# Kernel tuning notes

Hardware: AMD Instinct MI355X
Metric: run time of the kernel (lower is better)

Reference implementation:

```python
import jax, jax.numpy as jnp
import numpy as np

N, C_IN, F = 64, 1024, 20          # batch, backbone channels, grid size (640/32)
N_CLASSES = 80
A = 3                               # anchors in this layer (mask [6,7,8])
STRIDE = 32
C = N_CLASSES + 5                   # 85
C_OUT = A * C                       # 255
ANCHORS = np.array([[116.0, 90.0], [156.0, 198.0], [373.0, 326.0]], np.float32) / STRIDE


def setup_inputs() -> dict:
    key = jax.random.key(0)
    k1, k2 = jax.random.split(key)
    xin = jax.random.normal(k1, (N, C_IN, F, F), jnp.float32)
    conv_w = jax.random.normal(k2, (C_OUT, C_IN, 1, 1), jnp.float32) * 0.02
    conv_b = jnp.zeros((C_OUT,), jnp.float32)
    return {"xin": xin, "conv_w": conv_w, "conv_b": conv_b}


def reference(xin, conv_w, conv_b):
    anchors = jnp.asarray(ANCHORS, dtype=xin.dtype)  # [A, 2], grid units
    # 1x1 conv head: [N, C_OUT, F, F]
    out = jax.lax.conv_general_dilated(xin, conv_w, window_strides=(1, 1),
                                       padding="VALID")
    out = out + conv_b[None, :, None, None]
    # [N, A, C, F, F] -> [N, A, F(y), F(x), C]
    out = out.reshape(N, A, C, F, F).transpose(0, 1, 3, 4, 2)

    xy = jax.nn.sigmoid(out[..., :2])       # sigmoid on tx, ty
    wh = out[..., 2:4]                      # raw tw, th
    objcls = jax.nn.sigmoid(out[..., 4:])   # sigmoid on obj + classes

    grid = jnp.arange(F, dtype=xin.dtype)
    px = xy[..., 0] + grid[None, None, None, :]   # + x_shift (varies along last spatial dim)
    py = xy[..., 1] + grid[None, None, :, None]   # + y_shift
    pw = jnp.exp(wh[..., 0]) * anchors[:, 0].reshape(1, A, 1, 1)
    ph = jnp.exp(wh[..., 1]) * anchors[:, 1].reshape(1, A, 1, 1)

    boxes = jnp.stack([px, py, pw, ph], axis=-1) * STRIDE  # back to pixel coords
    pred = jnp.concatenate([boxes, objcls], axis=-1)       # [N, A, F, F, C]
    return pred.reshape(N, -1, C)                           # [N, A*F*F, C]
```

## Files before the change

kernel.cpp:

```cpp
#include <hip/hip_runtime.h>
#include <hip/hip_bf16.h>
#include <math.h>

#define CIN    1024
#define S_TOT  400
#define COUT   255
#define NCH    85
#define NIMG   64
#define BM     256
#define BN     80
#define BK     64
#define NSTEP  (CIN / BK)
#define NTHR   512

#define XS_BASE   32768
#define LDS_BYTES (32768 + 10240)
#define WSTEP_B   32768

typedef __attribute__((ext_vector_type(8))) short bf16x8;
typedef __attribute__((ext_vector_type(4))) float f32x4;

__device__ __forceinline__ int wOff(int co, int kg) {
    return (co << 7) + ((kg << 4) ^ ((co & 7) << 4));
}
__device__ __forceinline__ int xOff(int s, int kg) {
    return XS_BASE + (s << 7) + ((kg << 4) ^ (((s >> 1) & 7) << 4));
}

__device__ __forceinline__ unsigned pk2(float a, float b) {
    __hip_bfloat162 h;
    h.x = __float2bfloat16(a);
    h.y = __float2bfloat16(b);
    return *reinterpret_cast<unsigned*>(&h);
}

__device__ __forceinline__ float sigmoidf_(float v) {
    return 1.0f / (1.0f + expf(-v));
}

__device__ __forceinline__ void gload_lds16(const void* g, void* l) {
    __builtin_amdgcn_global_load_lds(
        (const __attribute__((address_space(1))) unsigned int*)g,
        (__attribute__((address_space(3))) unsigned int*)l,
        16, 0, 0);
}

__global__ __launch_bounds__(256) void w_pre(const float* __restrict__ w,
                                             unsigned short* __restrict__ wbf) {
    int g = blockIdx.x * 256 + threadIdx.x;
    int co    = g >> 7;
    int kgAll = g & 127;
    int k     = kgAll << 3;
    int step  = k >> 6;
    int kg    = (k >> 3) & 7;
    union { unsigned short u[8]; bf16x8 v; } pk;
    if (co < COUT) {
        const float* src = w + co * CIN + k;
        #pragma unroll
        for (int j = 0; j < 8; ++j) {
            __hip_bfloat16 h = __float2bfloat16(src[j]);
            pk.u[j] = *reinterpret_cast<unsigned short*>(&h);
        }
    } else {
        #pragma unroll
        for (int j = 0; j < 8; ++j) pk.u[j] = 0;
    }
    char* dst = reinterpret_cast<char*>(wbf) + step * WSTEP_B + wOff(co, kg);
    *reinterpret_cast<bf16x8*>(dst) = pk.v;
}

__global__ __launch_bounds__(NTHR) void yolo_mfma(
    const float* __restrict__ xin,
    const unsigned short* __restrict__ wbf,
    const float* __restrict__ bias,
    float* __restrict__ out)
{
    __shared__ __align__(16) char smem[LDS_BYTES];

    const int n     = blockIdx.y;
    const int sbase = blockIdx.x * BN;
    const int tid   = threadIdx.x;
    const int lane  = tid & 63;
    const int wid   = tid >> 6;

    const float* xin_n = xin + (size_t)n * (CIN * S_TOT);

    const bool xstage = tid < 320;
    const int  sp = tid % 40;
    const int  kg = tid / 40;
    const int  s0 = sp * 2;
    const float* xsrc0 = xin_n + (kg * 8) * S_TOT + sbase + s0;

    f32x4 acc[2][5] = {};

    float2 cur[8], nxt[8];
    if (xstage) {
        #pragma unroll
        for (int j = 0; j < 8; ++j) cur[j] = *(const float2*)(xsrc0 + j * S_TOT);
    }

    const int co_w = wid * 32;
    const int llo  = lane & 15;
    const int lhi  = lane >> 4;

    for (int t = 0; t < NSTEP; ++t) {
        const char* wg = (const char*)wbf + (size_t)t * WSTEP_B;
        #pragma unroll
        for (int i = 0; i < 4; ++i) {
            gload_lds16(wg + i * 8192 + (size_t)tid * 16,
                        smem + i * 8192 + wid * 1024);
        }

        if (xstage) {
            union { unsigned u[4]; bf16x8 v; } r0, r1;
            #pragma unroll
            for (int j = 0; j < 4; ++j) {
                r0.u[j] = pk2(cur[2 * j].x, cur[2 * j + 1].x);
                r1.u[j] = pk2(cur[2 * j].y, cur[2 * j + 1].y);
            }
            *(bf16x8*)(smem + xOff(s0,     kg)) = r0.v;
            *(bf16x8*)(smem + xOff(s0 + 1, kg)) = r1.v;
        }
        __syncthreads();

        if (t + 1 < NSTEP && xstage) {
            const float* src = xsrc0 + (t + 1) * BK * S_TOT;
            #pragma unroll
            for (int j = 0; j < 8; ++j) nxt[j] = *(const float2*)(src + j * S_TOT);
        }

        #pragma unroll
        for (int ks = 0; ks < 2; ++ks) {
            const int kgr = ks * 4 + lhi;
            bf16x8 a0 = *(bf16x8*)(smem + wOff(co_w + llo,      kgr));
            bf16x8 a1 = *(bf16x8*)(smem + wOff(co_w + 16 + llo, kgr));
            #pragma unroll
            for (int ni = 0; ni < 5; ++ni) {
                bf16x8 b = *(bf16x8*)(smem + xOff(ni * 16 + llo, kgr));
                acc[0][ni] = __builtin_amdgcn_mfma_f32_16x16x32_bf16(a0, b, acc[0][ni], 0, 0, 0);
                acc[1][ni] = __builtin_amdgcn_mfma_f32_16x16x32_bf16(a1, b, acc[1][ni], 0, 0, 0);
            }
        }
        __syncthreads();

        if (xstage) {
            #pragma unroll
            for (int j = 0; j < 8; ++j) cur[j] = nxt[j];
        }
    }

    const float anchW[3] = {116.0f, 156.0f, 373.0f};
    const float anchH[3] = {90.0f, 198.0f, 326.0f};

    #pragma unroll
    for (int mi = 0; mi < 2; ++mi) {
        #pragma unroll
        for (int r = 0; r < 4; ++r) {
            int co = co_w + mi * 16 + lhi * 4 + r;
            if (co < COUT) {
                int a = co / NCH;
                int c = co - a * NCH;
                float bv = bias[co];
                #pragma unroll
                for (int ni = 0; ni < 5; ++ni) {
                    int s = sbase + ni * 16 + llo;
                    float v = acc[mi][ni][r] + bv;
                    float res;
                    if (c == 0)      res = (sigmoidf_(v) + (float)(s % 20)) * 32.0f;
                    else if (c == 1) res = (sigmoidf_(v) + (float)(s / 20)) * 32.0f;
                    else if (c == 2) res = expf(v) * anchW[a];
                    else if (c == 3) res = expf(v) * anchH[a];
                    else             res = sigmoidf_(v);
                    out[(size_t)n * 102000 + a * 34000 + s * 85 + c] = res;
                }
            }
        }
    }
}

extern "C" void kernel_launch(void* const* d_in, const int* in_sizes, int n_in,
                              void* d_out, int out_size, void* d_ws, size_t ws_size,
                              hipStream_t stream) {
    const float* xin  = (const float*)d_in[0];
    const float* w    = (const float*)d_in[1];
    const float* bias = (const float*)d_in[2];
    float* out = (float*)d_out;
    unsigned short* wbf = (unsigned short*)d_ws;

    w_pre<<<128, 256, 0, stream>>>(w, wbf);
    yolo_mfma<<<dim3(S_TOT / BN, NIMG), NTHR, 0, stream>>>(xin, wbf, bias, out);
}
```

Measured before the change: 74.03 us.

## Double-buffer weight tiles in LDS and prefetch activations two steps ahead

The K loop is unrolled by two and uses two LDS weight buffers. The async global-to-LDS weight load for the next step is issued before the current step computes, and activation registers are prefetched two steps ahead in alternating register sets. Manual vmcnt/lgkmcnt waits and raw s_barrier calls replace __syncthreads, and launch bounds add an occupancy hint. The aim is to hide global load latency behind the MFMA work. In exchange the kernel uses more LDS and registers, which may reduce resident blocks per CU, and it depends on hand-counted outstanding-load numbers being right.

```diff
diff --git a/kernel.cpp b/kernel.cpp
--- a/kernel.cpp
+++ b/kernel.cpp
@@ -7,15 +7,16 @@
 #define COUT   255
 #define NCH    85
 #define NIMG   64
-#define BM     256
 #define BN     80
 #define BK     64
-#define NSTEP  (CIN / BK)
+#define NSTEP  16
 #define NTHR   512
 
-#define XS_BASE   32768
-#define LDS_BYTES (32768 + 10240)
-#define WSTEP_B   32768
+#define WB0      0
+#define WB1      32768
+#define XS_BASE  65536
+#define LDS_BYTES (65536 + 10240)
+#define WSTEP_B  32768
 
 typedef __attribute__((ext_vector_type(8))) short bf16x8;
 typedef __attribute__((ext_vector_type(4))) float f32x4;
@@ -69,7 +70,52 @@
     *reinterpret_cast<bf16x8*>(dst) = pk.v;
 }
 
-__global__ __launch_bounds__(NTHR) void yolo_mfma(
+#define PHASE(T, CURB, NXTB, RC)                                               \
+  {                                                                            \
+    __builtin_amdgcn_sched_barrier(0);                                         \
+    const int tn  = ((T) + 1 < NSTEP) ? (T) + 1 : NSTEP - 1;                   \
+    const int tn2 = ((T) + 2 < NSTEP) ? (T) + 2 : NSTEP - 1;                   \
+    const char* wg_ = (const char*)wbf + (size_t)tn * WSTEP_B;                 \
+    _Pragma("unroll")                                                          \
+    for (int i = 0; i < 4; ++i)                                                \
+      gload_lds16(wg_ + i * 8192 + (size_t)tid * 16,                           \
+                  smem + (NXTB) + i * 8192 + wid * 1024);                      \
+    __builtin_amdgcn_sched_barrier(0);                                         \
+    if (xstage) {                                                              \
+      union { unsigned u[4]; bf16x8 v; } r0_, r1_;                             \
+      _Pragma("unroll")                                                        \
+      for (int j = 0; j < 4; ++j) {                                            \
+        r0_.u[j] = pk2(RC[2 * j].x, RC[2 * j + 1].x);                          \
+        r1_.u[j] = pk2(RC[2 * j].y, RC[2 * j + 1].y);                          \
+      }                                                                        \
+      *(bf16x8*)(smem + xOff(s0, kg))     = r0_.v;                             \
+      *(bf16x8*)(smem + xOff(s0 + 1, kg)) = r1_.v;                             \
+      const float* xs_ = xsrc0 + (size_t)tn2 * (BK * S_TOT);                   \
+      _Pragma("unroll")                                                        \
+      for (int j = 0; j < 8; ++j) RC[j] = *(const float2*)(xs_ + j * S_TOT);   \
+    }                                                                          \
+    asm volatile("s_waitcnt lgkmcnt(0)" ::: "memory");                         \
+    if (xstage) asm volatile("s_waitcnt vmcnt(20)" ::: "memory");              \
+    else        asm volatile("s_waitcnt vmcnt(4)"  ::: "memory");              \
+    __builtin_amdgcn_s_barrier();                                              \
+    __builtin_amdgcn_sched_barrier(0);                                         \
+    _Pragma("unroll")                                                          \
+    for (int ks = 0; ks < 2; ++ks) {                                           \
+      const int kgr = ks * 4 + lhi;                                            \
+      bf16x8 a0 = *(bf16x8*)(smem + (CURB) + wOff(co_w + llo,      kgr));      \
+      bf16x8 a1 = *(bf16x8*)(smem + (CURB) + wOff(co_w + 16 + llo, kgr));      \
+      _Pragma("unroll")                                                        \
+      for (int ni = 0; ni < 5; ++ni) {                                         \
+        bf16x8 b = *(bf16x8*)(smem + xOff(ni * 16 + llo, kgr));                \
+        acc[0][ni] = __builtin_amdgcn_mfma_f32_16x16x32_bf16(a0, b, acc[0][ni], 0, 0, 0); \
+        acc[1][ni] = __builtin_amdgcn_mfma_f32_16x16x32_bf16(a1, b, acc[1][ni], 0, 0, 0); \
+      }                                                                        \
+    }                                                                          \
+    __builtin_amdgcn_sched_barrier(0);                                         \
+    __builtin_amdgcn_s_barrier();                                              \
+  }
+
+__global__ __launch_bounds__(NTHR, 4) void yolo_mfma(
     const float* __restrict__ xin,
     const unsigned short* __restrict__ wbf,
     const float* __restrict__ bias,
@@ -93,59 +139,40 @@
 
     f32x4 acc[2][5] = {};
 
-    float2 cur[8], nxt[8];
-    if (xstage) {
-        #pragma unroll
-        for (int j = 0; j < 8; ++j) cur[j] = *(const float2*)(xsrc0 + j * S_TOT);
-    }
-
     const int co_w = wid * 32;
     const int llo  = lane & 15;
     const int lhi  = lane >> 4;
 
-    for (int t = 0; t < NSTEP; ++t) {
-        const char* wg = (const char*)wbf + (size_t)t * WSTEP_B;
-        #pragma unroll
-        for (int i = 0; i < 4; ++i) {
-            gload_lds16(wg + i * 8192 + (size_t)tid * 16,
-                        smem + i * 8192 + wid * 1024);
-        }
-
-        if (xstage) {
-            union { unsigned u[4]; bf16x8 v; } r0, r1;
-            #pragma unroll
-            for (int j = 0; j < 4; ++j) {
-                r0.u[j] = pk2(cur[2 * j].x, cur[2 * j + 1].x);
-                r1.u[j] = pk2(cur[2 * j].y, cur[2 * j + 1].y);
-            }
-            *(bf16x8*)(smem + xOff(s0,     kg)) = r0.v;
-            *(bf16x8*)(smem + xOff(s0 + 1, kg)) = r1.v;
-        }
-        __syncthreads();
-
-        if (t + 1 < NSTEP && xstage) {
-            const float* src = xsrc0 + (t + 1) * BK * S_TOT;
-            #pragma unroll
-            for (int j = 0; j < 8; ++j) nxt[j] = *(const float2*)(src + j * S_TOT);
-        }
-
-        #pragma unroll
-        for (int ks = 0; ks < 2; ++ks) {
-            const int kgr = ks * 4 + lhi;
-            bf16x8 a0 = *(bf16x8*)(smem + wOff(co_w + llo,      kgr));
-            bf16x8 a1 = *(bf16x8*)(smem + wOff(co_w + 16 + llo, kgr));
-            #pragma unroll
-            for (int ni = 0; ni < 5; ++ni) {
-                bf16x8 b = *(bf16x8*)(smem + xOff(ni * 16 + llo, kgr));
-                acc[0][ni] = __builtin_amdgcn_mfma_f32_16x16x32_bf16(a0, b, acc[0][ni], 0, 0, 0);
-                acc[1][ni] = __builtin_amdgcn_mfma_f32_16x16x32_bf16(a1, b, acc[1][ni], 0, 0, 0);
-            }
-        }
-        __syncthreads();
-
-        if (xstage) {
-            #pragma unroll
-            for (int j = 0; j < 8; ++j) cur[j] = nxt[j];
+    float2 XE[8], XO[8];
+    if (xstage) {
+        #pragma unroll
+        for (int j = 0; j < 8; ++j) XE[j] = *(const float2*)(xsrc0 + j * S_TOT);
+    }
+    __builtin_amdgcn_sched_barrier(0);
+    {
+        const char* wg_ = (const char*)wbf;
+        #pragma unroll
+        for (int i = 0; i < 4; ++i)
+            gload_lds16(wg_ + i * 8192 + (size_t)tid * 16,
+                        smem + WB0 + i * 8192 + wid * 1024);
+    }
+    __builtin_amdgcn_sched_barrier(0);
+    if (xstage) {
+        const float* xs1 = xsrc0 + BK * S_TOT;
+        #pragma unroll
+        for (int j = 0; j < 8; ++j) XO[j] = *(const float2*)(xs1 + j * S_TOT);
+    }
+
+    for (int it = 0; it < NSTEP; it += 2) {
+        PHASE(it,     WB0, WB1, XE);
+        PHASE(it + 1, WB1, WB0, XO);
+    }
+
+    if (xstage) {
+        #pragma unroll
+        for (int j = 0; j < 8; ++j) {
+            asm volatile("" :: "v"(XE[j].x), "v"(XE[j].y));
+            asm volatile("" :: "v"(XO[j].x), "v"(XO[j].y));
         }
     }
 
```

After: 70.05 us. 5.4% less time.

## Split output channels across two blocks and vectorize epilogue stores

Applied to the files above, without the earlier changes.

The 255 output channels are split across two blocks of 256 threads each, replacing one 512-thread block that owned all channels, and launch bounds ask for 4 blocks per CU. The register double-buffering of the activation tile is dropped in favour of direct load-convert-store each step. The epilogue writes four consecutive channels with one 16-byte store when they fall in the same anchor. The aim is more resident blocks and fewer scattered stores. The cost is that every activation tile is read twice, and global load latency is no longer overlapped within the block.

```diff
diff --git a/kernel.cpp b/kernel.cpp
--- a/kernel.cpp
+++ b/kernel.cpp
@@ -7,18 +7,19 @@
 #define COUT   255
 #define NCH    85
 #define NIMG   64
-#define BM     256
 #define BN     80
 #define BK     64
-#define NSTEP  (CIN / BK)
-#define NTHR   512
-
-#define XS_BASE   32768
-#define LDS_BYTES (32768 + 10240)
+#define NSTEP  16
+#define NTHR   256
+
+#define XS_BASE   16384
+#define LDS_BYTES (16384 + 10240)
 #define WSTEP_B   32768
 
 typedef __attribute__((ext_vector_type(8))) short bf16x8;
 typedef __attribute__((ext_vector_type(4))) float f32x4;
+
+struct __attribute__((aligned(4))) f4u { float x, y, z, w; };
 
 __device__ __forceinline__ int wOff(int co, int kg) {
     return (co << 7) + ((kg << 4) ^ ((co & 7) << 4));
@@ -69,7 +70,21 @@
     *reinterpret_cast<bf16x8*>(dst) = pk.v;
 }
 
-__global__ __launch_bounds__(NTHR) void yolo_mfma(
+__device__ __forceinline__ void stageX(const float* base, char* smem, int s0, int kg) {
+    float2 cu[8];
+    #pragma unroll
+    for (int j = 0; j < 8; ++j) cu[j] = *(const float2*)(base + j * S_TOT);
+    union { unsigned u[4]; bf16x8 v; } r0, r1;
+    #pragma unroll
+    for (int j = 0; j < 4; ++j) {
+        r0.u[j] = pk2(cu[2 * j].x, cu[2 * j + 1].x);
+        r1.u[j] = pk2(cu[2 * j].y, cu[2 * j + 1].y);
+    }
+    *(bf16x8*)(smem + xOff(s0,     kg)) = r0.v;
+    *(bf16x8*)(smem + xOff(s0 + 1, kg)) = r1.v;
+}
+
+__global__ __launch_bounds__(NTHR, 4) void yolo_mfma(
     const float* __restrict__ xin,
     const unsigned short* __restrict__ wbf,
     const float* __restrict__ bias,
@@ -77,7 +92,8 @@
 {
     __shared__ __align__(16) char smem[LDS_BYTES];
 
-    const int n     = blockIdx.y;
+    const int n     = blockIdx.z;
+    const int cob   = blockIdx.y * 128;
     const int sbase = blockIdx.x * BN;
     const int tid   = threadIdx.x;
     const int lane  = tid & 63;
@@ -85,49 +101,31 @@
 
     const float* xin_n = xin + (size_t)n * (CIN * S_TOT);
 
-    const bool xstage = tid < 320;
-    const int  sp = tid % 40;
-    const int  kg = tid / 40;
-    const int  s0 = sp * 2;
-    const float* xsrc0 = xin_n + (kg * 8) * S_TOT + sbase + s0;
+    const int kg0 = tid / 40;
+    const int sp0 = tid % 40;
+    const int kg1 = (256 + tid) / 40;
+    const int sp1 = (256 + tid) % 40;
+    const bool dual = tid < 64;
 
     f32x4 acc[2][5] = {};
-
-    float2 cur[8], nxt[8];
-    if (xstage) {
-        #pragma unroll
-        for (int j = 0; j < 8; ++j) cur[j] = *(const float2*)(xsrc0 + j * S_TOT);
-    }
 
     const int co_w = wid * 32;
     const int llo  = lane & 15;
     const int lhi  = lane >> 4;
 
     for (int t = 0; t < NSTEP; ++t) {
-        const char* wg = (const char*)wbf + (size_t)t * WSTEP_B;
-        #pragma unroll
-        for (int i = 0; i < 4; ++i) {
-            gload_lds16(wg + i * 8192 + (size_t)tid * 16,
-                        smem + i * 8192 + wid * 1024);
-        }
-
-        if (xstage) {
-            union { unsigned u[4]; bf16x8 v; } r0, r1;
-            #pragma unroll
-            for (int j = 0; j < 4; ++j) {
-                r0.u[j] = pk2(cur[2 * j].x, cur[2 * j + 1].x);
-                r1.u[j] = pk2(cur[2 * j].y, cur[2 * j + 1].y);
-            }
-            *(bf16x8*)(smem + xOff(s0,     kg)) = r0.v;
-            *(bf16x8*)(smem + xOff(s0 + 1, kg)) = r1.v;
-        }
+        const char* wg = (const char*)wbf + (size_t)t * WSTEP_B + (size_t)cob * 128;
+        #pragma unroll
+        for (int i = 0; i < 4; ++i)
+            gload_lds16(wg + i * 4096 + (size_t)tid * 16,
+                        smem + i * 4096 + wid * 1024);
+
+        const float* xt = xin_n + (size_t)t * (BK * S_TOT) + sbase;
+        stageX(xt + kg0 * 8 * S_TOT + 2 * sp0, smem, 2 * sp0, kg0);
+        if (dual)
+            stageX(xt + kg1 * 8 * S_TOT + 2 * sp1, smem, 2 * sp1, kg1);
+
         __syncthreads();
-
-        if (t + 1 < NSTEP && xstage) {
-            const float* src = xsrc0 + (t + 1) * BK * S_TOT;
-            #pragma unroll
-            for (int j = 0; j < 8; ++j) nxt[j] = *(const float2*)(src + j * S_TOT);
-        }
 
         #pragma unroll
         for (int ks = 0; ks < 2; ++ks) {
@@ -142,11 +140,6 @@
             }
         }
         __syncthreads();
-
-        if (xstage) {
-            #pragma unroll
-            for (int j = 0; j < 8; ++j) cur[j] = nxt[j];
-        }
     }
 
     const float anchW[3] = {116.0f, 156.0f, 373.0f};
@@ -154,24 +147,53 @@
 
     #pragma unroll
     for (int mi = 0; mi < 2; ++mi) {
-        #pragma unroll
-        for (int r = 0; r < 4; ++r) {
-            int co = co_w + mi * 16 + lhi * 4 + r;
-            if (co < COUT) {
-                int a = co / NCH;
-                int c = co - a * NCH;
-                float bv = bias[co];
+        const int co0 = cob + co_w + mi * 16 + lhi * 4;
+        const int aW  = co0 / NCH;
+        const int c0  = co0 - aW * NCH;
+        const bool whole = (c0 <= NCH - 4) && (co0 + 3 < COUT);
+        float bv[4];
+        #pragma unroll
+        for (int r = 0; r < 4; ++r)
+            bv[r] = (co0 + r < COUT) ? bias[co0 + r] : 0.0f;
+
+        #pragma unroll
+        for (int ni = 0; ni < 5; ++ni) {
+            const int s  = sbase + ni * 16 + llo;
+            const float sx = (float)(s % 20);
+            const float sy = (float)(s / 20);
+            if (whole) {
+                float r4[4];
                 #pragma unroll
-                for (int ni = 0; ni < 5; ++ni) {
-                    int s = sbase + ni * 16 + llo;
-                    float v = acc[mi][ni][r] + bv;
+                for (int r = 0; r < 4; ++r) {
+                    const int c = c0 + r;
+                    const float v = acc[mi][ni][r] + bv[r];
                     float res;
-                    if (c == 0)      res = (sigmoidf_(v) + (float)(s % 20)) * 32.0f;
-                    else if (c == 1) res = (sigmoidf_(v) + (float)(s / 20)) * 32.0f;
-                    else if (c == 2) res = expf(v) * anchW[a];
-                    else if (c == 3) res = expf(v) * anchH[a];
+                    if (c == 0)      res = (sigmoidf_(v) + sx) * 32.0f;
+                    else if (c == 1) res = (sigmoidf_(v) + sy) * 32.0f;
+                    else if (c == 2) res = expf(v) * anchW[aW];
+                    else if (c == 3) res = expf(v) * anchH[aW];
                     else             res = sigmoidf_(v);
-                    out[(size_t)n * 102000 + a * 34000 + s * 85 + c] = res;
+                    r4[r] = res;
+                }
+                f4u* p = (f4u*)(out + (size_t)n * 102000 + aW * 34000 + s * 85 + c0);
+                f4u val = {r4[0], r4[1], r4[2], r4[3]};
+                *p = val;
+            } else {
+                #pragma unroll
+                for (int r = 0; r < 4; ++r) {
+                    const int co = co0 + r;
+                    if (co < COUT) {
+                        const int a2 = co / NCH;
+                        const int c  = co - a2 * NCH;
+                        const float v = acc[mi][ni][r] + bv[r];
+                        float res;
+                        if (c == 0)      res = (sigmoidf_(v) + sx) * 32.0f;
+                        else if (c == 1) res = (sigmoidf_(v) + sy) * 32.0f;
+                        else if (c == 2) res = expf(v) * anchW[a2];
+                        else if (c == 3) res = expf(v) * anchH[a2];
+                        else             res = sigmoidf_(v);
+                        out[(size_t)n * 102000 + a2 * 34000 + s * 85 + c] = res;
+                    }
                 }
             }
         }
@@ -188,5 +210,5 @@
     unsigned short* wbf = (unsigned short*)d_ws;
 
     w_pre<<<128, 256, 0, stream>>>(w, wbf);
-    yolo_mfma<<<dim3(S_TOT / BN, NIMG), NTHR, 0, stream>>>(xin, wbf, bias, out);
-}
+    yolo_mfma<<<dim3(S_TOT / BN, 2, NIMG), NTHR, 0, stream>>>(xin, wbf, bias, out);
+}
```

After: 68.94 us. 1.07x faster.
